# Kernel tuning notes

Measured on AMD Instinct MI355X. Metric: run time of the kernel, lower is better.

The kernel has to match this reference:

```python
import jax, jax.numpy as jnp
import numpy as np

D_MODEL = 2048
H_Q = 16
H_KV = 4
D_HEAD = D_MODEL // H_Q  # 128
G = H_Q // H_KV          # 4
B, S = 4, 2048


def setup_inputs() -> dict:
    key = jax.random.key(0)
    k1, k2, k3 = jax.random.split(key, 3)
    x = jax.random.normal(k1, (B, S, D_MODEL), dtype=jnp.float32)
    mask = jnp.zeros((S, S), dtype=jnp.float32)  # additive mask (zeros == no masking)
    # Linear weights, torch layout [out_features, in_features], bias=False
    Wqkv = jax.random.normal(k2, ((H_Q + 2 * H_KV) * D_HEAD, D_MODEL), dtype=jnp.float32) * (1.0 / np.sqrt(D_MODEL))
    Wo = jax.random.normal(k3, (D_MODEL, D_MODEL), dtype=jnp.float32) * (1.0 / np.sqrt(D_MODEL))
    return {"x": x, "mask": mask, "Wqkv": Wqkv, "Wo": Wo}


def reference(x, mask, Wqkv, Wo):
    d_q = H_Q * D_HEAD
    d_kv = H_KV * D_HEAD
    # fused QKV projection (Linear, no bias): x @ Wqkv.T
    qkv = jnp.einsum('bsd,ed->bse', x, Wqkv)  # [B,S,(H_Q+2*H_KV)*D_HEAD]
    q, k, v = jnp.split(qkv, [d_q, d_q + d_kv], axis=-1)
    q = q.reshape(B, S, H_Q, D_HEAD)
    k = k.reshape(B, S, H_KV, D_HEAD)
    v = v.reshape(B, S, H_KV, D_HEAD)
    # GQA: repeat_interleave KV heads G times along head axis
    k = jnp.repeat(k, G, axis=-2)  # [B,S,H_Q,D_HEAD]
    v = jnp.repeat(v, G, axis=-2)
    scale = 1.0 / np.sqrt(D_HEAD).astype(np.float32)
    scores = jnp.einsum('bqhd,bkhd->bhqk', q, k) * scale + mask  # [B,H_Q,S,S]
    attn = jax.nn.softmax(scores, axis=-1)
    out = jnp.einsum('bhqk,bkhd->bqhd', attn, v)  # [B,S,H_Q,D_HEAD]
    out = out.reshape(B, S, D_MODEL)
    return jnp.einsum('bsd,ed->bse', out, Wo)  # output projection
```

## Files before the change

### kernel.cpp

```cpp
#include <hip/hip_runtime.h>

#define D_MODEL 2048
#define S_LEN 2048
#define HQ 16
#define HKV 4
#define DH 128
#define QKV_W 3072
#define M_TOK 8192

typedef unsigned short u16;
typedef __bf16 bf16x8 __attribute__((ext_vector_type(8)));
typedef float f32x4 __attribute__((ext_vector_type(4)));
typedef float f32x16 __attribute__((ext_vector_type(16)));

__device__ __forceinline__ u16 f2bf(float f) {
  union { float f; unsigned u; } v; v.f = f;
  unsigned u = v.u;
  return (u16)((u + 0x7fffu + ((u >> 16) & 1u)) >> 16);
}

__device__ __forceinline__ bf16x8 ld_frag(const u16* p) {
  bf16x8 r; __builtin_memcpy(&r, p, 16); return r;
}

__device__ __forceinline__ void gl_lds16(const u16* g, u16* l) {
  __builtin_amdgcn_global_load_lds(
      (const __attribute__((address_space(1))) void*)g,
      (__attribute__((address_space(3))) void*)l, 16, 0, 0);
}

__device__ __forceinline__ unsigned cvtpk(float lo, float hi_) {
  unsigned r;
  asm("v_cvt_pk_bf16_f32 %0, %1, %2" : "=v"(r) : "v"(lo), "v"(hi_));
  return r;
}

__device__ __forceinline__ float exp2a(float x) {
  float r; asm("v_exp_f32 %0, %1" : "=v"(r) : "v"(x)); return r;
}

__device__ __forceinline__ float fmax3(float a, float b, float c) {
  float r;
  asm("v_max3_f32 %0, %1, %2, %3" : "=v"(r) : "v"(a), "v"(b), "v"(c));
  return r;
}

#define MFMA(a, b, c) __builtin_amdgcn_mfma_f32_16x16x32_bf16(a, b, c, 0, 0, 0)
#define MFMA32(a, b, c) __builtin_amdgcn_mfma_f32_32x32x16_bf16(a, b, c, 0, 0, 0)

__device__ __forceinline__ float vmax16(const f32x16& v) {
  float a = fmax3(v[0], v[1], v[2]);
  float b = fmax3(v[3], v[4], v[5]);
  float c = fmax3(v[6], v[7], v[8]);
  float d = fmax3(v[9], v[10], v[11]);
  float e = fmax3(v[12], v[13], v[14]);
  float f_ = fmax3(a, b, v[15]);
  float g = fmax3(c, d, e);
  return fmaxf(f_, g);
}

__global__ __launch_bounds__(256) void k_f32_to_bf16(const float* __restrict__ s,
                                                     u16* __restrict__ d,
                                                     long scale_n) {
  long i = (long)(blockIdx.x * 256 + threadIdx.x) * 8;
  float sc = (i < scale_n) ? 0.12751879677296637f : 1.0f;
  float a[8];
  __builtin_memcpy(a, s + i, 32);
  u16 r[8];
#pragma unroll
  for (int j = 0; j < 8; ++j) r[j] = f2bf(a[j] * sc);
  __builtin_memcpy(d + i, r, 16);
}

template <int OUT_BF16>
__global__ __launch_bounds__(512, 2) void k_gemm8p(const u16* __restrict__ A,
                                                   const u16* __restrict__ B,
                                                   void* __restrict__ C,
                                                   int M, int N, int K) {
  extern __shared__ __attribute__((aligned(16))) u16 S[];
  const int tid = threadIdx.x;
  const int lane = tid & 63;
  const int wid = tid >> 6;
  const int l15 = lane & 15, l4 = lane >> 4;
  const int wr = wid >> 2, wc = wid & 3;

  const int xcd = blockIdx.x & 7;
  const int slot = blockIdx.x >> 3;
  const long tm = (long)(xcd * 4 + (slot & 3)) * 256;
  const long tn = (long)(slot >> 2) * 256;

  f32x4 acc[8][4] = {};
  bf16x8 af[4], bfr[8];

#define STG_HT(g, sl)                                                       \
  do {                                                                      \
    const u16* src_ = ((sl) < 2) ? A : B;                                   \
    long rb_ = ((sl) < 2) ? (tm + (sl) * 128) : (tn + ((sl) - 2) * 128);    \
    u16* dst_ = S + (((g) & 1) * 4 + (sl)) * 8192;                          \
    _Pragma("unroll") for (int j = 0; j < 2; ++j) {                         \
      int q = tid + j * 512;                                                \
      int row = q >> 3, c = q & 7;                                          \
      int gg = c ^ (row & 7);                                               \
      gl_lds16(src_ + (rb_ + row) * (long)K + (long)(g) * 64 + gg * 8,      \
               dst_ + q * 8);                                               \
    }                                                                       \
  } while (0)

#define DSR_B(g)                                                            \
  {                                                                         \
    const u16* bs_ = S + (((g) & 1) * 4 + 2 + (wc >> 1)) * 8192 +           \
                     ((wc & 1) * 64) * 64;                                  \
    _Pragma("unroll") for (int n = 0; n < 4; ++n)                           \
        _Pragma("unroll") for (int k = 0; k < 2; ++k)                       \
            bfr[n * 2 + k] = ld_frag(bs_ + (n * 16 + l15) * 64 +            \
                                     (((k * 4 + l4) ^ (l15 & 7)) * 8));     \
  }
#define DSR_A(g, mp)                                                        \
  {                                                                         \
    const u16* as_ = S + (((g) & 1) * 4 + wr) * 8192;                       \
    _Pragma("unroll") for (int m = 0; m < 2; ++m)                           \
        _Pragma("unroll") for (int k = 0; k < 2; ++k)                       \
            af[m * 2 + k] = ld_frag(as_ + (((mp) * 2 + m) * 16 + l15) * 64 +\
                                    (((k * 4 + l4) ^ (l15 & 7)) * 8));      \
  }
#define MMQ(mp)                                                             \
  _Pragma("unroll") for (int m = 0; m < 2; ++m)                             \
      _Pragma("unroll") for (int n = 0; n < 4; ++n)                         \
          _Pragma("unroll") for (int k = 0; k < 2; ++k)                     \
              acc[(mp) * 2 + m][n] =                                        \
                  MFMA(af[m * 2 + k], bfr[n * 2 + k], acc[(mp) * 2 + m][n]);
#define LGKM0                                              \
  asm volatile("s_waitcnt lgkmcnt(0)" ::: "memory");       \
  __builtin_amdgcn_sched_barrier(0)
#define PRIO1 __builtin_amdgcn_s_setprio(1)
#define PRIO0 __builtin_amdgcn_s_setprio(0)
#define BAR __builtin_amdgcn_s_barrier()

  const int NT = K >> 6;
  STG_HT(0, 0); STG_HT(0, 1); STG_HT(0, 2); STG_HT(0, 3);
  STG_HT(1, 2); STG_HT(1, 3);
  asm volatile("s_waitcnt vmcnt(4)" ::: "memory");
  BAR;

  for (int g = 0; g < NT; ++g) {
    const bool s1 = (g + 1 < NT), s2 = (g + 2 < NT);
    DSR_B(g); DSR_A(g, 0);
    if (s1) STG_HT(g + 1, 0);
    BAR;
    LGKM0;
    PRIO1; MMQ(0); PRIO0;
    BAR;
    DSR_A(g, 1);
    if (s1) STG_HT(g + 1, 1);
    BAR;
    LGKM0;
    PRIO1; MMQ(1); PRIO0;
    BAR;
    DSR_A(g, 2);
    if (s2) STG_HT(g + 2, 2);
    BAR;
    LGKM0;
    PRIO1; MMQ(2); PRIO0;
    BAR;
    DSR_A(g, 3);
    if (s2) STG_HT(g + 2, 3);
    BAR;
    LGKM0;
    PRIO1; MMQ(3); PRIO0;
    if (s2) {
      asm volatile("s_waitcnt vmcnt(4)" ::: "memory");
    } else if (s1) {
      asm volatile("s_waitcnt vmcnt(0)" ::: "memory");
    }
    BAR;
  }
#undef STG_HT
#undef DSR_B
#undef DSR_A
#undef MMQ
#undef LGKM0
#undef PRIO1
#undef PRIO0
#undef BAR

#pragma unroll
  for (int mf = 0; mf < 8; ++mf)
#pragma unroll
    for (int n = 0; n < 4; ++n)
#pragma unroll
      for (int i = 0; i < 4; ++i) {
        long row = tm + wr * 128 + mf * 16 + l4 * 4 + i;
        long col = tn + wc * 64 + n * 16 + l15;
        if (OUT_BF16)
          ((u16*)C)[row * N + col] = f2bf(acc[mf][n][i]);
        else
          ((float*)C)[row * N + col] = acc[mf][n][i];
      }
}

__global__ __launch_bounds__(256) void k_vtrans(const u16* __restrict__ qkv,
                                                u16* __restrict__ vt) {
  __shared__ u16 T[64][68];
  const int tid = threadIdx.x;
  const int st = blockIdx.x;
  const int dt = blockIdx.y;
  const int bh = blockIdx.z;
  const int b = bh >> 2, kvh = bh & 3;
  const long s0 = (long)st * 64, d0 = (long)dt * 64;
#pragma unroll
  for (int j = 0; j < 2; ++j) {
    int chunk = tid + j * 256;
    int row = chunk >> 3, c8 = chunk & 7;
    u16 tmp[8];
    __builtin_memcpy(tmp,
                     qkv + ((long)b * S_LEN + s0 + row) * QKV_W + 2560 +
                         kvh * DH + d0 + c8 * 8,
                     16);
    __builtin_memcpy(&T[row][c8 * 8], tmp, 16);
  }
  __syncthreads();
#pragma unroll
  for (int j = 0; j < 2; ++j) {
    int chunk = tid + j * 256;
    int drow = chunk >> 3, c8 = chunk & 7;
    u16 tmp[8];
#pragma unroll
    for (int e = 0; e < 8; ++e) tmp[e] = T[c8 * 8 + e][drow];
    __builtin_memcpy(vt + ((long)bh * DH + d0 + drow) * S_LEN + s0 + c8 * 8,
                     tmp, 16);
  }
}

__global__ __launch_bounds__(512, 2) void k_attn(const u16* __restrict__ qkv,
                                                 const u16* __restrict__ vt,
                                                 u16* __restrict__ ao) {
  __shared__ __attribute__((aligned(16))) u16 Ks[2][8192];
  __shared__ __attribute__((aligned(16))) u16 Vs[2][8192];
  const int tid = threadIdx.x;
  const int lane = tid & 63;
  const int wid = tid >> 6;
  const int l31 = lane & 31, hi = lane >> 5;
  const int xcd = blockIdx.x & 7;
  const int s = blockIdx.x >> 3;
  const int bkv = (xcd << 1) | (s & 1);
  const int hh = (s >> 1) & 3;
  const int qt = (s >> 3) & 7;
  const int b = bkv >> 2, kvh = bkv & 3;
  const int h = kvh * 4 + hh;
  const long rowbase = (long)b * S_LEN;
  const int q0 = qt * 256 + wid * 32;
  const long vbase = (long)bkv * DH * S_LEN;

  bf16x8 qf[8];
  {
    const u16* qrow = qkv + (rowbase + q0 + l31) * QKV_W + h * DH;
#pragma unroll
    for (int kk = 0; kk < 8; ++kk) qf[kk] = ld_frag(qrow + kk * 16 + hi * 8);
  }

  bf16x8 onesf;
  {
    union { u16 u[8]; bf16x8 v; } t;
#pragma unroll
    for (int e = 0; e < 8; ++e) t.u[e] = 0x3F80;
    onesf = t.v;
  }

  f32x16 o[4] = {};
  f32x16 osum = {};
  float m_run = -3.0e38f;

#define STAGE(KDST, VDST, tile)                                               \
  do {                                                                        \
    long s0_ = (long)(tile) * 64;                                             \
    _Pragma("unroll") for (int j = 0; j < 2; ++j) {                           \
      int chunk = (wid * 2 + j) * 64 + lane;                                  \
      int row = chunk >> 4, cc = chunk & 15;                                  \
      gl_lds16(qkv + (rowbase + s0_ + row) * QKV_W + 2048 + kvh * DH +        \
                   ((cc ^ (row & 7)) * 8),                                    \
               &(KDST)[chunk * 8]);                                           \
    }                                                                         \
    _Pragma("unroll") for (int j = 0; j < 2; ++j) {                           \
      int chunk = (wid * 2 + j) * 64 + lane;                                  \
      int row = chunk >> 3, cc = chunk & 7;                                   \
      gl_lds16(vt + vbase + (long)row * S_LEN + s0_ + ((cc ^ (row & 7)) * 8), \
               &(VDST)[chunk * 8]);                                           \
    }                                                                         \
  } while (0)

#define PROCESS(KSP, VSP)                                                     \
  {                                                                           \
    f32x16 p0 = {}, p1 = {};                                                  \
    __builtin_amdgcn_s_setprio(1);                                            \
    _Pragma("unroll") for (int kk = 0; kk < 8; ++kk) {                        \
      int ch0 = ((2 * kk + hi) ^ (l31 & 7));                                  \
      int ch1 = ((2 * kk + hi) ^ ((l31 + 32) & 7));                           \
      bf16x8 kf0 = ld_frag((KSP) + l31 * 128 + ch0 * 8);                      \
      bf16x8 kf1 = ld_frag((KSP) + (32 + l31) * 128 + ch1 * 8);               \
      p0 = MFMA32(kf0, qf[kk], p0);                                           \
      p1 = MFMA32(kf1, qf[kk], p1);                                           \
    }                                                                         \
    __builtin_amdgcn_s_setprio(0);                                            \
    float mx = fmaxf(vmax16(p0), vmax16(p1));                                 \
    mx = fmaxf(mx, __shfl_xor(mx, 32, 64));                                   \
    if (__any(mx > m_run + 11.0f)) {                                          \
      float nm = fmaxf(m_run, mx);                                            \
      float alpha = exp2a(m_run - nm);                                        \
      m_run = nm;                                                             \
      _Pragma("unroll") for (int r = 0; r < 16; ++r) osum[r] *= alpha;        \
      _Pragma("unroll") for (int n2 = 0; n2 < 4; ++n2)                        \
          _Pragma("unroll") for (int r = 0; r < 16; ++r) o[n2][r] *= alpha;   \
    }                                                                         \
    _Pragma("unroll") for (int r = 0; r < 16; ++r) {                          \
      p0[r] = exp2a(p0[r] - m_run);                                           \
      p1[r] = exp2a(p1[r] - m_run);                                           \
    }                                                                         \
    __builtin_amdgcn_s_setprio(1);                                            \
    _Pragma("unroll") for (int ks_ = 0; ks_ < 4; ++ks_) {                     \
      const f32x16& pp = (ks_ < 2) ? p0 : p1;                                 \
      const int bb = 8 * (ks_ & 1);                                           \
      unsigned A0 = cvtpk(pp[bb + 0], pp[bb + 1]);                            \
      unsigned A1 = cvtpk(pp[bb + 2], pp[bb + 3]);                            \
      unsigned B0 = cvtpk(pp[bb + 4], pp[bb + 5]);                            \
      unsigned B1 = cvtpk(pp[bb + 6], pp[bb + 7]);                            \
      asm volatile("v_permlane32_swap_b32 %0, %1" : "+v"(A0), "+v"(B0));      \
      asm volatile("v_permlane32_swap_b32 %0, %1" : "+v"(A1), "+v"(B1));      \
      union { unsigned u[4]; bf16x8 v; } pu;                                  \
      pu.u[0] = A0; pu.u[1] = A1; pu.u[2] = B0; pu.u[3] = B1;                 \
      osum = MFMA32(onesf, pu.v, osum);                                       \
      _Pragma("unroll") for (int n2 = 0; n2 < 4; ++n2) {                      \
        int vr = n2 * 32 + l31;                                               \
        int ch = ((2 * ks_ + hi) ^ (vr & 7));                                 \
        bf16x8 vf = ld_frag((VSP) + vr * 64 + ch * 8);                        \
        o[n2] = MFMA32(vf, pu.v, o[n2]);                                      \
      }                                                                       \
    }                                                                         \
    __builtin_amdgcn_s_setprio(0);                                            \
  }

  STAGE(Ks[0], Vs[0], 0);

  for (int kt2 = 0; kt2 < 16; ++kt2) {
    const bool tail = (kt2 == 15);
    STAGE(Ks[1], Vs[1], 2 * kt2 + 1);
    asm volatile("s_waitcnt vmcnt(4)" ::: "memory");
    __builtin_amdgcn_s_barrier();
    PROCESS(&Ks[0][0], &Vs[0][0]);
    __builtin_amdgcn_s_barrier();
    if (!tail) {
      STAGE(Ks[0], Vs[0], 2 * kt2 + 2);
      asm volatile("s_waitcnt vmcnt(4)" ::: "memory");
    } else {
      asm volatile("s_waitcnt vmcnt(0)" ::: "memory");
    }
    __builtin_amdgcn_s_barrier();
    PROCESS(&Ks[1][0], &Vs[1][0]);
    __builtin_amdgcn_s_barrier();
  }

  {
    float inv = 1.0f / osum[0];
    u16* orow = ao + (rowbase + q0 + l31) * D_MODEL + h * DH;
#pragma unroll
    for (int n2 = 0; n2 < 4; ++n2)
#pragma unroll
      for (int g = 0; g < 4; ++g) {
        u16 tmp[4];
#pragma unroll
        for (int e = 0; e < 4; ++e) tmp[e] = f2bf(o[n2][g * 4 + e] * inv);
        __builtin_memcpy(orow + n2 * 32 + g * 8 + 4 * hi, tmp, 8);
      }
  }
#undef STAGE
#undef PROCESS
}

extern "C" void kernel_launch(void* const* d_in, const int* in_sizes, int n_in,
                              void* d_out, int out_size, void* d_ws,
                              size_t ws_size, hipStream_t stream) {
  const float* x = (const float*)d_in[0];
  const float* wqkv = (const float*)d_in[2];
  const float* wo = (const float*)d_in[3];
  char* ws = (char*)d_ws;
  u16* xb = (u16*)(ws);
  u16* wqkvb = (u16*)(ws + 33554432);
  u16* wob = (u16*)(ws + 46137344);
  u16* qkv = (u16*)(ws + 54525952);
  u16* vt = (u16*)(ws + 104857600);
  u16* ao = xb;

  hipFuncSetAttribute(reinterpret_cast<const void*>(k_gemm8p<1>),
                      hipFuncAttributeMaxDynamicSharedMemorySize, 131072);
  hipFuncSetAttribute(reinterpret_cast<const void*>(k_gemm8p<0>),
                      hipFuncAttributeMaxDynamicSharedMemorySize, 131072);

  k_f32_to_bf16<<<8192, 256, 0, stream>>>(x, xb, 0);
  k_f32_to_bf16<<<3072, 256, 0, stream>>>(wqkv, wqkvb, 4194304L);
  k_f32_to_bf16<<<2048, 256, 0, stream>>>(wo, wob, 0);
  k_gemm8p<1><<<384, 512, 131072, stream>>>(xb, wqkvb, qkv, M_TOK, QKV_W,
                                            D_MODEL);
  k_vtrans<<<dim3(32, 2, 16), 256, 0, stream>>>(qkv, vt);
  k_attn<<<512, 512, 0, stream>>>(qkv, vt, ao);
  k_gemm8p<0><<<256, 512, 131072, stream>>>(ao, wob, d_out, M_TOK, D_MODEL,
                                            D_MODEL);
}
```

Baseline: 373.1 us.

## Software-pipeline attention so QK^T of tile T overlaps PV of tile T-1

Restructures the flash-attention inner loop so each iteration computes QK^T for the current KV tile while doing the P·V MFMAs for the previous tile, using packed bf16 probabilities kept in registers. K and V staging are split so the V buffer of the previous tile is refilled only after its PV step has finished. The online-softmax rescale is deferred by one tile. The aim is to hide softmax/exp latency and global-load waits behind MFMA work, at the cost of more live registers (16 packed P values plus the deferred alpha) and different barrier and waitcnt placement.

```diff
diff --git a/kernel.cpp b/kernel.cpp
--- a/kernel.cpp
+++ b/kernel.cpp
@@ -269,8 +269,11 @@
   f32x16 o[4] = {};
   f32x16 osum = {};
   float m_run = -3.0e38f;
-
-#define STAGE(KDST, VDST, tile)                                               \
+  float alpha_p = 1.0f;
+  int need_p = 0;
+  unsigned pa[16];
+
+#define STAGE_K(KDST, tile)                                                   \
   do {                                                                        \
     long s0_ = (long)(tile) * 64;                                             \
     _Pragma("unroll") for (int j = 0; j < 2; ++j) {                           \
@@ -280,6 +283,10 @@
                    ((cc ^ (row & 7)) * 8),                                    \
                &(KDST)[chunk * 8]);                                           \
     }                                                                         \
+  } while (0)
+#define STAGE_V(VDST, tile)                                                   \
+  do {                                                                        \
+    long s0_ = (long)(tile) * 64;                                             \
     _Pragma("unroll") for (int j = 0; j < 2; ++j) {                           \
       int chunk = (wid * 2 + j) * 64 + lane;                                  \
       int row = chunk >> 3, cc = chunk & 7;                                   \
@@ -288,45 +295,13 @@
     }                                                                         \
   } while (0)
 
-#define PROCESS(KSP, VSP)                                                     \
+#define PVSTEP(VSP)                                                           \
   {                                                                           \
-    f32x16 p0 = {}, p1 = {};                                                  \
-    __builtin_amdgcn_s_setprio(1);                                            \
-    _Pragma("unroll") for (int kk = 0; kk < 8; ++kk) {                        \
-      int ch0 = ((2 * kk + hi) ^ (l31 & 7));                                  \
-      int ch1 = ((2 * kk + hi) ^ ((l31 + 32) & 7));                           \
-      bf16x8 kf0 = ld_frag((KSP) + l31 * 128 + ch0 * 8);                      \
-      bf16x8 kf1 = ld_frag((KSP) + (32 + l31) * 128 + ch1 * 8);               \
-      p0 = MFMA32(kf0, qf[kk], p0);                                           \
-      p1 = MFMA32(kf1, qf[kk], p1);                                           \
-    }                                                                         \
-    __builtin_amdgcn_s_setprio(0);                                            \
-    float mx = fmaxf(vmax16(p0), vmax16(p1));                                 \
-    mx = fmaxf(mx, __shfl_xor(mx, 32, 64));                                   \
-    if (__any(mx > m_run + 11.0f)) {                                          \
-      float nm = fmaxf(m_run, mx);                                            \
-      float alpha = exp2a(m_run - nm);                                        \
-      m_run = nm;                                                             \
-      _Pragma("unroll") for (int r = 0; r < 16; ++r) osum[r] *= alpha;        \
-      _Pragma("unroll") for (int n2 = 0; n2 < 4; ++n2)                        \
-          _Pragma("unroll") for (int r = 0; r < 16; ++r) o[n2][r] *= alpha;   \
-    }                                                                         \
-    _Pragma("unroll") for (int r = 0; r < 16; ++r) {                          \
-      p0[r] = exp2a(p0[r] - m_run);                                           \
-      p1[r] = exp2a(p1[r] - m_run);                                           \
-    }                                                                         \
     __builtin_amdgcn_s_setprio(1);                                            \
     _Pragma("unroll") for (int ks_ = 0; ks_ < 4; ++ks_) {                     \
-      const f32x16& pp = (ks_ < 2) ? p0 : p1;                                 \
-      const int bb = 8 * (ks_ & 1);                                           \
-      unsigned A0 = cvtpk(pp[bb + 0], pp[bb + 1]);                            \
-      unsigned A1 = cvtpk(pp[bb + 2], pp[bb + 3]);                            \
-      unsigned B0 = cvtpk(pp[bb + 4], pp[bb + 5]);                            \
-      unsigned B1 = cvtpk(pp[bb + 6], pp[bb + 7]);                            \
-      asm volatile("v_permlane32_swap_b32 %0, %1" : "+v"(A0), "+v"(B0));      \
-      asm volatile("v_permlane32_swap_b32 %0, %1" : "+v"(A1), "+v"(B1));      \
       union { unsigned u[4]; bf16x8 v; } pu;                                  \
-      pu.u[0] = A0; pu.u[1] = A1; pu.u[2] = B0; pu.u[3] = B1;                 \
+      pu.u[0] = pa[ks_ * 4 + 0]; pu.u[1] = pa[ks_ * 4 + 1];                   \
+      pu.u[2] = pa[ks_ * 4 + 2]; pu.u[3] = pa[ks_ * 4 + 3];                   \
       osum = MFMA32(onesf, pu.v, osum);                                       \
       _Pragma("unroll") for (int n2 = 0; n2 < 4; ++n2) {                      \
         int vr = n2 * 32 + l31;                                               \
@@ -338,26 +313,82 @@
     __builtin_amdgcn_s_setprio(0);                                            \
   }
 
-  STAGE(Ks[0], Vs[0], 0);
-
-  for (int kt2 = 0; kt2 < 16; ++kt2) {
-    const bool tail = (kt2 == 15);
-    STAGE(Ks[1], Vs[1], 2 * kt2 + 1);
-    asm volatile("s_waitcnt vmcnt(4)" ::: "memory");
-    __builtin_amdgcn_s_barrier();
-    PROCESS(&Ks[0][0], &Vs[0][0]);
-    __builtin_amdgcn_s_barrier();
-    if (!tail) {
-      STAGE(Ks[0], Vs[0], 2 * kt2 + 2);
-      asm volatile("s_waitcnt vmcnt(4)" ::: "memory");
-    } else {
-      asm volatile("s_waitcnt vmcnt(0)" ::: "memory");
-    }
-    __builtin_amdgcn_s_barrier();
-    PROCESS(&Ks[1][0], &Vs[1][0]);
-    __builtin_amdgcn_s_barrier();
-  }
-
+#define RESCALE                                                               \
+  if (need_p) {                                                               \
+    _Pragma("unroll") for (int r = 0; r < 16; ++r) osum[r] *= alpha_p;        \
+    _Pragma("unroll") for (int n2 = 0; n2 < 4; ++n2)                          \
+        _Pragma("unroll") for (int r = 0; r < 16; ++r) o[n2][r] *= alpha_p;   \
+  }
+
+#define ITER(T, DO_PV, DO_STAGE)                                              \
+  {                                                                           \
+    if (DO_STAGE) STAGE_K(Ks[((T) + 1) & 1], (T) + 1);                        \
+    f32x16 p0 = {}, p1 = {};                                                  \
+    {                                                                         \
+      const u16* ksp = &Ks[(T) & 1][0];                                       \
+      __builtin_amdgcn_s_setprio(1);                                          \
+      _Pragma("unroll") for (int kk = 0; kk < 8; ++kk) {                      \
+        int ch0 = ((2 * kk + hi) ^ (l31 & 7));                                \
+        int ch1 = ((2 * kk + hi) ^ ((l31 + 32) & 7));                         \
+        bf16x8 kf0 = ld_frag(ksp + l31 * 128 + ch0 * 8);                      \
+        bf16x8 kf1 = ld_frag(ksp + (32 + l31) * 128 + ch1 * 8);               \
+        p0 = MFMA32(kf0, qf[kk], p0);                                         \
+        p1 = MFMA32(kf1, qf[kk], p1);                                         \
+      }                                                                       \
+      __builtin_amdgcn_s_setprio(0);                                          \
+    }                                                                         \
+    RESCALE;                                                                  \
+    if (DO_PV) PVSTEP(&Vs[((T) + 1) & 1][0]);         \
+    __builtin_amdgcn_s_barrier();                                             \
+    if (DO_STAGE) STAGE_V(Vs[((T) + 1) & 1], (T) + 1);                        \
+    {                                                                         \
+      float mx = fmaxf(vmax16(p0), vmax16(p1));                               \
+      mx = fmaxf(mx, __shfl_xor(mx, 32, 64));                                 \
+      need_p = __any(mx > m_run + 11.0f);                                     \
+      if (need_p) {                                                           \
+        float nm = fmaxf(m_run, mx);                                          \
+        alpha_p = exp2a(m_run - nm);                                          \
+        m_run = nm;                                                           \
+      }                                                                       \
+      _Pragma("unroll") for (int r = 0; r < 16; ++r) {                        \
+        p0[r] = exp2a(p0[r] - m_run);                                         \
+        p1[r] = exp2a(p1[r] - m_run);                                         \
+      }                                                                       \
+      _Pragma("unroll") for (int ks_ = 0; ks_ < 4; ++ks_) {                   \
+        const f32x16& pp = (ks_ < 2) ? p0 : p1;                               \
+        const int bb = 8 * (ks_ & 1);                                         \
+        unsigned A0 = cvtpk(pp[bb + 0], pp[bb + 1]);                          \
+        unsigned A1 = cvtpk(pp[bb + 2], pp[bb + 3]);                          \
+        unsigned B0 = cvtpk(pp[bb + 4], pp[bb + 5]);                          \
+        unsigned B1 = cvtpk(pp[bb + 6], pp[bb + 7]);                          \
+        asm volatile("v_permlane32_swap_b32 %0, %1" : "+v"(A0), "+v"(B0));    \
+        asm volatile("v_permlane32_swap_b32 %0, %1" : "+v"(A1), "+v"(B1));    \
+        pa[ks_ * 4 + 0] = A0; pa[ks_ * 4 + 1] = A1;                           \
+        pa[ks_ * 4 + 2] = B0; pa[ks_ * 4 + 3] = B1;                           \
+      }                                                                       \
+    }                                                                         \
+    if (DO_STAGE) {                                                           \
+      asm volatile("s_waitcnt vmcnt(2)" ::: "memory");                        \
+    } else {                                                                  \
+      asm volatile("s_waitcnt vmcnt(0)" ::: "memory");                        \
+    }                                                                         \
+    __builtin_amdgcn_s_barrier();                                             \
+  }
+
+  STAGE_K(Ks[0], 0);
+  STAGE_V(Vs[0], 0);
+  asm volatile("s_waitcnt vmcnt(0)" ::: "memory");
+  __builtin_amdgcn_s_barrier();
+
+  ITER(0, false, true);
+  for (int k2 = 0; k2 < 15; ++k2) {
+    ITER(2 * k2 + 1, true, true);
+    ITER(2 * k2 + 2, true, true);
+  }
+  ITER(31, true, false);
+
+  RESCALE;
+  PVSTEP(&Vs[1][0]);
   {
     float inv = 1.0f / osum[0];
     u16* orow = ao + (rowbase + q0 + l31) * D_MODEL + h * DH;
@@ -371,8 +402,11 @@
         __builtin_memcpy(orow + n2 * 32 + g * 8 + 4 * hi, tmp, 8);
       }
   }
-#undef STAGE
-#undef PROCESS
+#undef STAGE_K
+#undef STAGE_V
+#undef PVSTEP
+#undef RESCALE
+#undef ITER
 }
 
 extern "C" void kernel_launch(void* const* d_in, const int* in_sizes, int n_in,
```

After: 383.1 us. 2.7% more time.
